# Optimization experiments

Hardware: AMD Instinct MI355X
Metric: run time of the kernel (lower is better)

The kernel has to match this reference:

```python
import jax, jax.numpy as jnp
import numpy as np

B, T, D, H, J = 64, 128, 768, 256, 128  # batch, tokens, input_dim, span_hidden_dim, top_injection_dim
PRUNING_RATIO = 2.0


def setup_inputs() -> dict:
    key = jax.random.key(0)
    ks = jax.random.split(key, 12)
    def w(k, shape, fan_in):
        return jax.random.normal(k, shape, jnp.float32) / np.sqrt(fan_in)
    return {
        "inputs": jax.random.normal(ks[0], (B, T, D), jnp.float32),
        "input_mask": jnp.ones((B, T), jnp.int32),
        "top_injection_embedding": jax.random.normal(ks[1], (B, J), jnp.float32),
        # SpanRepAssembly: start / end projections
        "W_start": w(ks[2], (D, H), D), "b_start": jnp.zeros((H,), jnp.float32),
        "W_end": w(ks[3], (D, H), D), "b_end": jnp.zeros((H,), jnp.float32),
        # span_scorer: ReLU -> Linear(H,H) -> ReLU -> Linear(H,1)
        "W_s1": w(ks[4], (H, H), H), "b_s1": jnp.zeros((H,), jnp.float32),
        "W_s2": w(ks[5], (H, 1), H), "b_s2": jnp.zeros((1,), jnp.float32),
        # top injection path
        "W_inj": w(ks[6], (J, H), J), "b_inj": jnp.zeros((H,), jnp.float32),
        "W_sec": w(ks[7], (H, H), H), "b_sec": jnp.zeros((H,), jnp.float32),
        "W_pred": w(ks[8], (H, 1), H), "b_pred": jnp.zeros((1,), jnp.float32),
    }


def reference(inputs, input_mask, top_injection_embedding,
              W_start, b_start, W_end, b_end,
              W_s1, b_s1, W_s2, b_s2,
              W_inj, b_inj, W_sec, b_sec, W_pred, b_pred):
    b, t, _ = inputs.shape
    k_spans = int(PRUNING_RATIO * t)
    # SpanRepAssembly: span_hidden[b, (s,e)] = startProj(x_s) + endProj(x_e), s <= e,
    # flattened start-major (matches start_end_range ordering).
    A = inputs @ W_start + b_start                      # [B,T,H]
    E = inputs @ W_end + b_end                          # [B,T,H]
    s_idx, e_idx = jnp.triu_indices(t)                  # N = T(T+1)/2 spans, row-major
    span_hidden = A[:, s_idx] + E[:, e_idx]             # [B,N,H]
    m = input_mask.astype(jnp.float32)
    span_mask = m[:, s_idx] * m[:, e_idx]               # [B,N]
    # span_scorer MLP over all spans
    h = jax.nn.relu(span_hidden) @ W_s1 + b_s1
    scores = (jax.nn.relu(h) @ W_s2 + b_s2)[..., 0]     # [B,N]
    # SpanPruner: mask invalid spans to -inf, top-k, sort indices, gather
    masked_scores = jnp.where(span_mask > 0, scores, -jnp.inf)
    _, top_idx = jax.lax.top_k(masked_scores, k_spans)  # [B,K]
    top_idx = jnp.sort(top_idx, axis=1)
    top_span_hidden = jnp.take_along_axis(span_hidden, top_idx[:, :, None], axis=1)  # [B,K,H]
    top_span_mask = jnp.take_along_axis(span_mask, top_idx, axis=1)[..., None]       # [B,K,1]
    top_span_scores = jnp.take_along_axis(masked_scores, top_idx, axis=1)[..., None] # [B,K,1]
    top_span_scores = jnp.where(jnp.isinf(top_span_scores), -1.0, top_span_scores)
    # top-injection scoring head
    inj = (top_injection_embedding @ W_inj + b_inj)[:, None, :]      # [B,1,H]
    sec = top_span_hidden @ W_sec + b_sec                            # [B,K,H]
    top_span_logits = jax.nn.relu(inj + sec) @ W_pred + b_pred + top_span_scores  # [B,K,1]
    top_span_probs = jax.nn.sigmoid(top_span_logits) * top_span_mask
    return top_span_probs
```

## Files before the change

### kernel.cpp

```cpp
#include <hip/hip_runtime.h>
#include <hip/hip_bf16.h>
#include <math.h>

#define BB 64
#define T 128
#define DD 768
#define H 256
#define JJ 128
#define NSPAN 8256
#define KTOP 256
#define SCAP 1024
#define MARGIN 0.03f

typedef __attribute__((ext_vector_type(8))) short bf16x8;
typedef __attribute__((ext_vector_type(4))) float f32x4;

__device__ inline unsigned short bfrne(float x) {
    unsigned u = __float_as_uint(x);
    return (unsigned short)((u + 0x7FFFu + ((u >> 16) & 1u)) >> 16);
}

__device__ inline unsigned pk2(float x, float y) {
    float2 f; f.x = x; f.y = y;
    __hip_bfloat162 h = __float22bfloat162_rn(f);
    return *reinterpret_cast<unsigned*>(&h);
}

template<int CTRL>
__device__ __forceinline__ float dpp_add16(float v) {
    return v + __int_as_float(__builtin_amdgcn_update_dpp(
        0, __float_as_int(v), CTRL, 0xF, 0xF, true));
}

__global__ __launch_bounds__(256) void prep_proj_kernel(
    const float* __restrict__ X,
    const float* __restrict__ Wa, const float* __restrict__ ba,
    const float* __restrict__ Wb, const float* __restrict__ bb,
    float* __restrict__ AE,
    int* __restrict__ s_idx, int* __restrict__ e_idx,
    const float* __restrict__ W1, unsigned short* __restrict__ Wpk,
    const float* __restrict__ tie, const float* __restrict__ Winj,
    const float* __restrict__ binj, float* __restrict__ injv)
{
    const int blk = blockIdx.x;
    const int t = threadIdx.x;

    if (blk >= 256) {
        const int pblk = blk - 256;
        if (pblk == 0) {
            if (t < T) {
                int s = t;
                int start = s * T - (s * (s - 1)) / 2;
                int len = T - s;
                for (int i = 0; i < len; ++i) {
                    s_idx[start + i] = s;
                    e_idx[start + i] = s + i;
                }
            }
        } else if (pblk <= 256) {
            int idx = (pblk - 1) * 256 + t;
            int j  = idx & 7;
            int l  = (idx >> 3) & 63;
            int kc = (idx >> 9) & 7;
            int ct = idx >> 12;
            int k = kc * 32 + (l >> 4) * 8 + j;
            int n = ct * 16 + (l & 15);
            Wpk[idx] = bfrne(W1[k * 256 + n]);
        } else {
            int b = pblk - 257;
            __shared__ float tb[JJ];
            if (t < JJ) tb[t] = tie[b * JJ + t];
            __syncthreads();
            float a = binj[t];
            for (int j = 0; j < JJ; ++j)
                a = fmaf(tb[j], Winj[j * H + t], a);
            injv[b * H + t] = a;
        }
        return;
    }

    const int px = blk & 63;
    const int cb = blk >> 6;
    const int m0 = px * 128;
    const float* W    = (cb < 2) ? Wa : Wb;
    const float* bias = (cb < 2) ? ba : bb;
    const int wc0 = (cb & 1) * 128;
    const int oc0 = (cb < 2) ? wc0 : (256 + wc0);

    const int tx = t & 15;
    const int ty = t >> 4;
    const int r0 = m0 + ty * 8;
    const int c0 = wc0 + tx * 8;

    const float* Xb  = X + (size_t)r0 * DD;
    const float* Wc  = W + c0;

    float4 XA[8], WA[8], XB[8], WB[8];
    float acc[8][8];
#pragma unroll
    for (int i = 0; i < 8; ++i)
#pragma unroll
        for (int j = 0; j < 8; ++j) acc[i][j] = 0.f;

    auto loadX = [&](float4 (&xr)[8], int kb) {
        const int kk = kb * 4;
#pragma unroll
        for (int r = 0; r < 8; ++r)
            xr[r] = *(const float4*)&Xb[(size_t)r * DD + kk];
    };
    auto loadW = [&](float4 (&wr)[8], int kb) {
#pragma unroll
        for (int j = 0; j < 4; ++j) {
            const float* wp = &Wc[(size_t)(kb * 4 + j) * 256];
            wr[j * 2]     = *(const float4*)&wp[0];
            wr[j * 2 + 1] = *(const float4*)&wp[4];
        }
    };
    auto comp = [&](const float4 (&xr)[8], const float4 (&wr)[8]) {
#pragma unroll
        for (int j = 0; j < 4; ++j) {
            const float wq[8] = {wr[j*2].x, wr[j*2].y, wr[j*2].z, wr[j*2].w,
                                 wr[j*2+1].x, wr[j*2+1].y, wr[j*2+1].z, wr[j*2+1].w};
#pragma unroll
            for (int r = 0; r < 8; ++r) {
                const float xv = (j == 0) ? xr[r].x : (j == 1) ? xr[r].y
                               : (j == 2) ? xr[r].z : xr[r].w;
#pragma unroll
                for (int c = 0; c < 8; ++c)
                    acc[r][c] = fmaf(xv, wq[c], acc[r][c]);
            }
        }
    };

    loadX(XA, 0); loadW(WA, 0);
    for (int kb = 0; kb < 192; kb += 2) {
        loadX(XB, kb + 1); loadW(WB, kb + 1);
        comp(XA, WA);
        if (kb + 2 < 192) { loadX(XA, kb + 2); loadW(WA, kb + 2); }
        comp(XB, WB);
    }

    float bq[8];
#pragma unroll
    for (int j = 0; j < 8; ++j) bq[j] = bias[wc0 + tx * 8 + j];
#pragma unroll
    for (int r = 0; r < 8; ++r) {
        const size_t row = r0 + r;
        float4 o0, o1;
        o0.x = acc[r][0] + bq[0]; o0.y = acc[r][1] + bq[1];
        o0.z = acc[r][2] + bq[2]; o0.w = acc[r][3] + bq[3];
        o1.x = acc[r][4] + bq[4]; o1.y = acc[r][5] + bq[5];
        o1.z = acc[r][6] + bq[6]; o1.w = acc[r][7] + bq[7];
        *(float4*)&AE[row * 512 + oc0 + tx * 8]     = o0;
        *(float4*)&AE[row * 512 + oc0 + tx * 8 + 4] = o1;
    }
}

__global__ __launch_bounds__(512, 4) void approx_kernel(
    const float* __restrict__ AE,
    const unsigned short* __restrict__ Wpk,
    const float* __restrict__ bs1, const float* __restrict__ Ws2,
    const float* __restrict__ bs2g,
    const int* __restrict__ s_idx, const int* __restrict__ e_idx,
    const int* __restrict__ maskp,
    float* __restrict__ scores)
{
    const int bid   = blockIdx.x;
    const int r     = bid & 7;
    const int q     = bid >> 3;
    const int g     = q >> 3;
    const int chunk = q & 7;
    const int b     = g * 8 + r;
    const int tile0 = chunk * 65;
    const int tcnt  = (516 - tile0 < 65) ? (516 - tile0) : 65;

    __shared__ __align__(16) unsigned short rshf[2][8][64][8];
    __shared__ float pslice[2][8][16];

    const int t      = threadIdx.x;
    const int w      = t >> 6;
    const int lane   = t & 63;
    const int lrow16 = lane & 15;
    const int quad   = lane >> 4;

    bf16x8 bfr[2][8];
    float b1c[2], w2c[2];
#pragma unroll
    for (int c = 0; c < 2; ++c) {
#pragma unroll
        for (int kc = 0; kc < 8; ++kc)
            bfr[c][kc] = *(const bf16x8*)&Wpk[((((2 * w + c) * 8 + kc) * 64) + lane) * 8];
        int col = (2 * w + c) * 16 + lrow16;
        b1c[c] = bs1[col];
        w2c[c] = Ws2[col];
    }
    const float bs2v = bs2g[0];

    const float* Abase = AE + (size_t)b * T * 512;
    const int sp   = t >> 5;
    const int km   = t & 31;
    const int kc_s = km >> 2;
    const int q_s  = km & 3;
    const int slot = (q_s * 16 + sp + kc_s) & 63;

    {
        int n = tile0 * 16 + sp;
        int s = s_idx[n], e = e_idx[n];
        const float* Ar = Abase + (size_t)s * 512 + km * 8;
        const float* Er = Abase + (size_t)e * 512 + 256 + km * 8;
        float4 a0 = *(const float4*)&Ar[0];
        float4 a1 = *(const float4*)&Ar[4];
        float4 e0 = *(const float4*)&Er[0];
        float4 e1 = *(const float4*)&Er[4];
        uint4 v;
        v.x = pk2(fmaxf(a0.x + e0.x, 0.f), fmaxf(a0.y + e0.y, 0.f));
        v.y = pk2(fmaxf(a0.z + e0.z, 0.f), fmaxf(a0.w + e0.w, 0.f));
        v.z = pk2(fmaxf(a1.x + e1.x, 0.f), fmaxf(a1.y + e1.y, 0.f));
        v.w = pk2(fmaxf(a1.z + e1.z, 0.f), fmaxf(a1.w + e1.w, 0.f));
        *(uint4*)&rshf[0][kc_s][slot][0] = v;
    }
    int s_nx = 0, e_nx = 0;
    if (tcnt > 1) {
        int n = (tile0 + 1) * 16 + sp;
        s_nx = s_idx[n]; e_nx = e_idx[n];
    }
    __syncthreads();

    for (int tt = 0; tt < tcnt; ++tt) {
        const int cur = tt & 1;
        float4 a0, a1, e0, e1;
        const bool pf = (tt + 1 < tcnt);
        if (pf) {
            const float* Ar = Abase + (size_t)s_nx * 512 + km * 8;
            const float* Er = Abase + (size_t)e_nx * 512 + 256 + km * 8;
            a0 = *(const float4*)&Ar[0];
            a1 = *(const float4*)&Ar[4];
            e0 = *(const float4*)&Er[0];
            e1 = *(const float4*)&Er[4];
        }
        if (tt + 2 < tcnt) {
            int n = (tile0 + tt + 2) * 16 + sp;
            s_nx = s_idx[n]; e_nx = e_idx[n];
        }
        f32x4 acc0 = {0.f, 0.f, 0.f, 0.f};
        f32x4 acc1 = {0.f, 0.f, 0.f, 0.f};
#pragma unroll
        for (int kc = 0; kc < 8; ++kc) {
            bf16x8 a = *(const bf16x8*)&rshf[cur][kc][(lane + kc) & 63][0];
            acc0 = __builtin_amdgcn_mfma_f32_16x16x32_bf16(a, bfr[0][kc], acc0, 0, 0, 0);
            acc1 = __builtin_amdgcn_mfma_f32_16x16x32_bf16(a, bfr[1][kc], acc1, 0, 0, 0);
        }
        float ps[4];
#pragma unroll
        for (int rr = 0; rr < 4; ++rr)
            ps[rr] = fmaxf(acc0[rr] + b1c[0], 0.f) * w2c[0]
                   + fmaxf(acc1[rr] + b1c[1], 0.f) * w2c[1];
#pragma unroll
        for (int rr = 0; rr < 4; ++rr) {
            float v = ps[rr];
            v = dpp_add16<0xB1>(v);
            v = dpp_add16<0x4E>(v);
            v = dpp_add16<0x141>(v);
            v = dpp_add16<0x140>(v);
            ps[rr] = v;
        }
        if (lrow16 == 0) {
            float4 v; v.x = ps[0]; v.y = ps[1]; v.z = ps[2]; v.w = ps[3];
            *(float4*)&pslice[cur][w][quad * 4] = v;
        }
        if (pf) {
            uint4 v;
            v.x = pk2(fmaxf(a0.x + e0.x, 0.f), fmaxf(a0.y + e0.y, 0.f));
            v.y = pk2(fmaxf(a0.z + e0.z, 0.f), fmaxf(a0.w + e0.w, 0.f));
            v.z = pk2(fmaxf(a1.x + e1.x, 0.f), fmaxf(a1.y + e1.y, 0.f));
            v.w = pk2(fmaxf(a1.z + e1.z, 0.f), fmaxf(a1.w + e1.w, 0.f));
            *(uint4*)&rshf[cur ^ 1][kc_s][slot][0] = v;
        }
        __syncthreads();
        if (t < 16) {
            int n = (tile0 + tt) * 16 + t;
            float sc = bs2v;
#pragma unroll
            for (int ww = 0; ww < 8; ++ww) sc += pslice[cur][ww][t];
            int s = s_idx[n], e = e_idx[n];
            bool m = (maskp[b * T + s] != 0) && (maskp[b * T + e] != 0);
            scores[(size_t)b * NSPAN + n] = m ? sc : -INFINITY;
        }
    }
}

__global__ __launch_bounds__(1024) void select_kernel(
    const float* __restrict__ scores,
    int* __restrict__ shortlist, int* __restrict__ slcnt)
{
    const int b = blockIdx.x;
    const int t = threadIdx.x;
    __shared__ unsigned su[NSPAN];
    __shared__ int hist[256];
    __shared__ unsigned s_prefix;
    __shared__ int s_remaining;
    __shared__ int wave_keep[16];

    const float* sc = scores + (size_t)b * NSPAN;
    for (int i = t; i < NSPAN; i += 1024) {
        unsigned ub = __float_as_uint(sc[i]);
        su[i] = (ub & 0x80000000u) ? ~ub : (ub | 0x80000000u);
    }
    __syncthreads();

    unsigned prefix = 0;
    int remaining = KTOP;
    for (int d = 3; d >= 0; --d) {
        if (t < 256) hist[t] = 0;
        __syncthreads();
        const int sh = d * 8;
        for (int i = t; i < NSPAN; i += 1024) {
            unsigned u = su[i];
            bool match = (d == 3) || ((u >> (sh + 8)) == (prefix >> (sh + 8)));
            if (match) atomicAdd(&hist[(u >> sh) & 255], 1);
        }
        __syncthreads();
        if (t == 0) {
            int acc = 0, v = 255;
            for (; v > 0; --v) {
                int h = hist[v];
                if (acc + h >= remaining) break;
                acc += h;
            }
            s_prefix = prefix | ((unsigned)v << sh);
            s_remaining = remaining - acc;
        }
        __syncthreads();
        prefix = s_prefix;
        remaining = s_remaining;
        __syncthreads();
    }

    unsigned ub = (prefix & 0x80000000u) ? (prefix & 0x7FFFFFFFu) : ~prefix;
    float kthf = __uint_as_float(ub);
    float tau = kthf - MARGIN;
    unsigned tb = __float_as_uint(tau);
    unsigned ktau = (tb & 0x80000000u) ? ~tb : (tb | 0x80000000u);

    const int wid = t >> 6, lane = t & 63;
    int base = 0;
    const unsigned long long ltmask = (1ull << lane) - 1ull;
    for (int c0 = 0; c0 < NSPAN; c0 += 1024) {
        int n = c0 + t;
        bool keep = (n < NSPAN) && (su[n] >= ktau);
        unsigned long long bk = __ballot(keep);
        int before = __popcll(bk & ltmask);
        if (lane == 0) wave_keep[wid] = __popcll(bk);
        __syncthreads();
        int kb = base;
        for (int wv = 0; wv < wid; ++wv) kb += wave_keep[wv];
        if (keep) {
            int pos = kb + before;
            if (pos < SCAP) shortlist[b * SCAP + pos] = n;
        }
        for (int wv = 0; wv < 16; ++wv) base += wave_keep[wv];
        __syncthreads();
    }
    if (t == 0) slcnt[b] = base < SCAP ? base : SCAP;
}

__global__ __launch_bounds__(512) void exact_kernel(
    const float* __restrict__ AE,
    const float* __restrict__ Ws1, const float* __restrict__ bs1,
    const float* __restrict__ Ws2, const float* __restrict__ bs2g,
    const int* __restrict__ s_idx, const int* __restrict__ e_idx,
    const int* __restrict__ shortlist, const int* __restrict__ slcnt,
    float* __restrict__ scores)
{
    const int b  = blockIdx.y;
    const int n0 = blockIdx.x * 64;
    const int cntb = slcnt[b];
    if (n0 >= cntb) return;

    __shared__ float rsh[64][36];
    __shared__ float Ws[32][260];
    __shared__ int   ss[64], se[64], nn[64];

    const int t = threadIdx.x;
    if (t < 64) {
        int row = n0 + t;
        int n = 0;
        if (row < cntb) n = shortlist[b * SCAP + row];
        nn[t] = (row < cntb) ? n : -1;
        ss[t] = s_idx[n]; se[t] = e_idx[n];
    }
    __syncthreads();

    const int tx = t & 31;
    const int ty = t >> 5;
    float acc[4][8];
#pragma unroll
    for (int i = 0; i < 4; ++i)
#pragma unroll
        for (int j = 0; j < 8; ++j) acc[i][j] = 0.f;

    const float* Abase = AE + (size_t)b * T * 512;

    for (int kk = 0; kk < 256; kk += 32) {
        __syncthreads();
        {
            int row = t >> 4, q4 = (t & 15) * 4;
#pragma unroll
            for (int q = 0; q < 4; ++q)
                *(float4*)&Ws[row][q4 + q * 64] =
                    *(const float4*)&Ws1[(size_t)(kk + row) * 256 + q4 + q * 64];
        }
        {
            int sp = t >> 3, k4 = (t & 7) * 4;
            const float* Ar = Abase + (size_t)ss[sp] * 512 + kk + k4;
            const float* Er = Abase + (size_t)se[sp] * 512 + 256 + kk + k4;
            float4 a = *(const float4*)Ar;
            float4 e = *(const float4*)Er;
            float4 v;
            v.x = fmaxf(a.x + e.x, 0.f); v.y = fmaxf(a.y + e.y, 0.f);
            v.z = fmaxf(a.z + e.z, 0.f); v.w = fmaxf(a.w + e.w, 0.f);
            *(float4*)&rsh[sp][k4] = v;
        }
        __syncthreads();
#pragma unroll
        for (int k4 = 0; k4 < 32; k4 += 4) {
            float w[4][8];
#pragma unroll
            for (int kq = 0; kq < 4; ++kq) {
                float4 w0 = *(const float4*)&Ws[k4 + kq][tx * 4];
                float4 w1 = *(const float4*)&Ws[k4 + kq][128 + tx * 4];
                w[kq][0] = w0.x; w[kq][1] = w0.y; w[kq][2] = w0.z; w[kq][3] = w0.w;
                w[kq][4] = w1.x; w[kq][5] = w1.y; w[kq][6] = w1.z; w[kq][7] = w1.w;
            }
#pragma unroll
            for (int i = 0; i < 4; ++i) {
                float4 rv = *(const float4*)&rsh[ty * 4 + i][k4];
                float rq[4] = {rv.x, rv.y, rv.z, rv.w};
#pragma unroll
                for (int kq = 0; kq < 4; ++kq)
#pragma unroll
                    for (int j = 0; j < 8; ++j)
                        acc[i][j] = fmaf(rq[kq], w[kq][j], acc[i][j]);
            }
        }
    }

    float b1[8], w2[8];
#pragma unroll
    for (int j = 0; j < 8; ++j) {
        int c = (j < 4) ? (tx * 4 + j) : (128 + tx * 4 + j - 4);
        b1[j] = bs1[c];
        w2[j] = Ws2[c];
    }
    const float bs2v = bs2g[0];
#pragma unroll
    for (int i = 0; i < 4; ++i) {
        int r = ty * 4 + i;
        float p = 0.f;
#pragma unroll
        for (int j = 0; j < 8; ++j)
            p += fmaxf(acc[i][j] + b1[j], 0.f) * w2[j];
#pragma unroll
        for (int off = 16; off > 0; off >>= 1)
            p += __shfl_down(p, off, 32);
        if (tx == 0) {
            int n = nn[r];
            if (n >= 0)
                scores[(size_t)b * NSPAN + n] = p + bs2v;
        }
    }
}

__global__ __launch_bounds__(1024) void topk_kernel(
    const float* __restrict__ scores,
    const int* __restrict__ shortlist, const int* __restrict__ slcnt,
    int* __restrict__ top_idx, float* __restrict__ top_scores)
{
    const int b = blockIdx.x;
    const int t = threadIdx.x;
    const int cnt = slcnt[b];

    __shared__ unsigned su[SCAP];
    __shared__ int sn[SCAP];
    __shared__ int hist[256];
    __shared__ unsigned s_prefix;
    __shared__ int s_remaining;
    __shared__ int wave_eq[16], wave_keep[16];

    for (int i = t; i < cnt; i += 1024) {
        int n = shortlist[b * SCAP + i];
        unsigned ub = __float_as_uint(scores[(size_t)b * NSPAN + n]);
        su[i] = (ub & 0x80000000u) ? ~ub : (ub | 0x80000000u);
        sn[i] = n;
    }
    __syncthreads();

    unsigned prefix = 0;
    int remaining = KTOP;
    for (int d = 3; d >= 0; --d) {
        if (t < 256) hist[t] = 0;
        __syncthreads();
        const int sh = d * 8;
        for (int i = t; i < cnt; i += 1024) {
            unsigned u = su[i];
            bool match = (d == 3) || ((u >> (sh + 8)) == (prefix >> (sh + 8)));
            if (match) atomicAdd(&hist[(u >> sh) & 255], 1);
        }
        __syncthreads();
        if (t == 0) {
            int acc = 0, v = 255;
            for (; v > 0; --v) {
                int h = hist[v];
                if (acc + h >= remaining) break;
                acc += h;
            }
            s_prefix = prefix | ((unsigned)v << sh);
            s_remaining = remaining - acc;
        }
        __syncthreads();
        prefix = s_prefix;
        remaining = s_remaining;
        __syncthreads();
    }
    const unsigned v = prefix;
    const int need_eq = remaining;

    const int wid = t >> 6, lane = t & 63;
    int base_eq = 0, base_keep = 0;
    const unsigned long long ltmask = (1ull << lane) - 1ull;
    for (int c0 = 0; c0 < cnt; c0 += 1024) {
        int i = c0 + t;
        bool valid = i < cnt;
        unsigned u = valid ? su[i] : 0u;
        bool eq = valid && (u == v);
        bool gt = valid && (u > v);
        unsigned long long beq = __ballot(eq);
        int eq_before = __popcll(beq & ltmask);
        if (lane == 0) wave_eq[wid] = __popcll(beq);
        __syncthreads();
        int eqb = base_eq;
        for (int w = 0; w < wid; ++w) eqb += wave_eq[w];
        int eq_rank = eqb + eq_before;
        bool keep = gt || (eq && (eq_rank < need_eq));
        unsigned long long bk = __ballot(keep);
        int keep_before = __popcll(bk & ltmask);
        if (lane == 0) wave_keep[wid] = __popcll(bk);
        __syncthreads();
        int kb = base_keep;
        for (int w = 0; w < wid; ++w) kb += wave_keep[w];
        if (keep) {
            int pos = kb + keep_before;
            top_idx[b * KTOP + pos] = sn[i];
            unsigned fb = (u & 0x80000000u) ? (u & 0x7FFFFFFFu) : ~u;
            float f = __uint_as_float(fb);
            top_scores[b * KTOP + pos] = isinf(f) ? -1.0f : f;
        }
        for (int w = 0; w < 16; ++w) { base_eq += wave_eq[w]; base_keep += wave_keep[w]; }
        __syncthreads();
    }
}

__global__ __launch_bounds__(256) void final_kernel(
    const float* __restrict__ AE,
    const int* __restrict__ s_idx, const int* __restrict__ e_idx,
    const int* __restrict__ maskp,
    const int* __restrict__ top_idx, const float* __restrict__ top_scores,
    const float* __restrict__ injv,
    const float* __restrict__ Wsec, const float* __restrict__ bsec,
    const float* __restrict__ Wpred, const float* __restrict__ bpredg,
    float* __restrict__ out)
{
    const int b = blockIdx.x >> 2;
    const int k0 = (blockIdx.x & 3) * 64;

    __shared__ float sh[64][36];
    __shared__ float Ws[32][260];
    __shared__ int ss[64], se[64];
    __shared__ float msk[64], tsc[64];

    const int t = threadIdx.x;
    if (t < 64) {
        int kidx = k0 + t;
        int n = top_idx[b * KTOP + kidx];
        int s = s_idx[n], e = e_idx[n];
        ss[t] = s; se[t] = e;
        msk[t] = (maskp[b * T + s] != 0 && maskp[b * T + e] != 0) ? 1.f : 0.f;
        tsc[t] = top_scores[b * KTOP + kidx];
    }
    __syncthreads();

    const int tx = t & 31;
    const int ty = t >> 5;
    float acc[8][8];
#pragma unroll
    for (int i = 0; i < 8; ++i)
#pragma unroll
        for (int j = 0; j < 8; ++j) acc[i][j] = 0.f;

    const float* Abase = AE + (size_t)b * T * 512;

    for (int kk = 0; kk < 256; kk += 32) {
        __syncthreads();
        {
            int c4 = (t & 63) * 4, r0 = t >> 6;
#pragma unroll
            for (int r8 = 0; r8 < 8; ++r8) {
                int row = r0 + r8 * 4;
                *(float4*)&Ws[row][c4] =
                    *(const float4*)&Wsec[(size_t)(kk + row) * 256 + c4];
            }
        }
        {
            int sp = t >> 2, k8 = (t & 3) * 8;
            const float* Ar = Abase + (size_t)ss[sp] * 512 + kk + k8;
            const float* Er = Abase + (size_t)se[sp] * 512 + 256 + kk + k8;
#pragma unroll
            for (int q = 0; q < 2; ++q) {
                float4 a = *(const float4*)&Ar[q * 4];
                float4 e = *(const float4*)&Er[q * 4];
                float4 v;
                v.x = a.x + e.x; v.y = a.y + e.y; v.z = a.z + e.z; v.w = a.w + e.w;
                *(float4*)&sh[sp][k8 + q * 4] = v;
            }
        }
        __syncthreads();
#pragma unroll
        for (int k4 = 0; k4 < 32; k4 += 4) {
            float w[4][8];
#pragma unroll
            for (int kq = 0; kq < 4; ++kq) {
                float4 w0 = *(const float4*)&Ws[k4 + kq][tx * 4];
                float4 w1 = *(const float4*)&Ws[k4 + kq][128 + tx * 4];
                w[kq][0] = w0.x; w[kq][1] = w0.y; w[kq][2] = w0.z; w[kq][3] = w0.w;
                w[kq][4] = w1.x; w[kq][5] = w1.y; w[kq][6] = w1.z; w[kq][7] = w1.w;
            }
#pragma unroll
            for (int i = 0; i < 8; ++i) {
                float4 rv = *(const float4*)&sh[ty * 8 + i][k4];
                float rq[4] = {rv.x, rv.y, rv.z, rv.w};
#pragma unroll
                for (int kq = 0; kq < 4; ++kq)
#pragma unroll
                    for (int j = 0; j < 8; ++j)
                        acc[i][j] = fmaf(rq[kq], w[kq][j], acc[i][j]);
            }
        }
    }

    float bsec_r[8], wpred_r[8], injr[8];
#pragma unroll
    for (int j = 0; j < 8; ++j) {
        int c = (j < 4) ? (tx * 4 + j) : (128 + tx * 4 + j - 4);
        bsec_r[j] = bsec[c];
        wpred_r[j] = Wpred[c];
        injr[j] = injv[b * H + c];
    }
    const float bp = bpredg[0];
#pragma unroll
    for (int i = 0; i < 8; ++i) {
        int r = ty * 8 + i;
        float p = 0.f;
#pragma unroll
        for (int j = 0; j < 8; ++j) {
            float sec = acc[i][j] + bsec_r[j];
            p += fmaxf(injr[j] + sec, 0.f) * wpred_r[j];
        }
#pragma unroll
        for (int off = 16; off > 0; off >>= 1)
            p += __shfl_down(p, off, 32);
        if (tx == 0) {
            float logit = p + bp + tsc[r];
            float prob = (1.f / (1.f + expf(-logit))) * msk[r];
            out[b * KTOP + k0 + r] = prob;
        }
    }
}

extern "C" void kernel_launch(void* const* d_in, const int* in_sizes, int n_in,
                              void* d_out, int out_size, void* d_ws, size_t ws_size,
                              hipStream_t stream) {
    const float* inputs  = (const float*)d_in[0];
    const int*   imask   = (const int*)d_in[1];
    const float* tie     = (const float*)d_in[2];
    const float* W_start = (const float*)d_in[3];
    const float* b_start = (const float*)d_in[4];
    const float* W_end   = (const float*)d_in[5];
    const float* b_end   = (const float*)d_in[6];
    const float* W_s1    = (const float*)d_in[7];
    const float* b_s1    = (const float*)d_in[8];
    const float* W_s2    = (const float*)d_in[9];
    const float* b_s2    = (const float*)d_in[10];
    const float* W_inj   = (const float*)d_in[11];
    const float* b_inj   = (const float*)d_in[12];
    const float* W_sec   = (const float*)d_in[13];
    const float* b_sec   = (const float*)d_in[14];
    const float* W_pred  = (const float*)d_in[15];
    const float* b_pred  = (const float*)d_in[16];
    float* out = (float*)d_out;

    float* AE         = (float*)d_ws;
    float* scores     = AE + (size_t)BB * T * 512;
    int*   s_idx      = (int*)(scores + (size_t)BB * NSPAN);
    int*   e_idx      = s_idx + NSPAN;
    int*   top_idx    = e_idx + NSPAN;
    float* top_scores = (float*)(top_idx + BB * KTOP);
    float* injv       = top_scores + BB * KTOP;
    unsigned short* Wpk = (unsigned short*)(injv + BB * H);
    int*   shortlist  = (int*)(Wpk + 65536);
    int*   slcnt      = shortlist + BB * SCAP;

    prep_proj_kernel<<<577, 256, 0, stream>>>(inputs, W_start, b_start, W_end, b_end, AE,
                                              s_idx, e_idx, W_s1, Wpk,
                                              tie, W_inj, b_inj, injv);
    approx_kernel<<<512, 512, 0, stream>>>(AE, Wpk, b_s1, W_s2, b_s2,
                                           s_idx, e_idx, imask, scores);
    select_kernel<<<BB, 1024, 0, stream>>>(scores, shortlist, slcnt);
    exact_kernel<<<dim3(16, BB), 512, 0, stream>>>(AE, W_s1, b_s1, W_s2, b_s2,
                                                   s_idx, e_idx, shortlist, slcnt, scores);
    topk_kernel<<<BB, 1024, 0, stream>>>(scores, shortlist, slcnt, top_idx, top_scores);
    final_kernel<<<BB * 4, 256, 0, stream>>>(AE, s_idx, e_idx, imask, top_idx, top_scores,
                                             injv, W_sec, b_sec, W_pred, b_pred, out);
}
```

Measured before the change: 477.7 us.

## Stage projection weights in shared memory and halve the column tile per block

Result: slower. 591.1 us (+23.7%).

```diff
diff --git a/kernel.cpp b/kernel.cpp
--- a/kernel.cpp
+++ b/kernel.cpp
@@ -45,8 +45,8 @@
     const int blk = blockIdx.x;
     const int t = threadIdx.x;
 
-    if (blk >= 256) {
-        const int pblk = blk - 256;
+    if (blk >= 512) {
+        const int pblk = blk - 512;
         if (pblk == 0) {
             if (t < T) {
                 int s = t;
@@ -80,79 +80,91 @@
     }
 
     const int px = blk & 63;
-    const int cb = blk >> 6;
+    const int cw = blk >> 6;
     const int m0 = px * 128;
-    const float* W    = (cb < 2) ? Wa : Wb;
-    const float* bias = (cb < 2) ? ba : bb;
-    const int wc0 = (cb & 1) * 128;
-    const int oc0 = (cb < 2) ? wc0 : (256 + wc0);
+    const float* W    = (cw < 4) ? Wa : Wb;
+    const float* bias = (cw < 4) ? ba : bb;
+    const int c0w = (cw & 3) * 64;
+    const int oc0 = (cw < 4) ? c0w : (256 + c0w);
 
     const int tx = t & 15;
     const int ty = t >> 4;
     const int r0 = m0 + ty * 8;
-    const int c0 = wc0 + tx * 8;
-
-    const float* Xb  = X + (size_t)r0 * DD;
-    const float* Wc  = W + c0;
-
-    float4 XA[8], WA[8], XB[8], WB[8];
-    float acc[8][8];
-#pragma unroll
-    for (int i = 0; i < 8; ++i)
-#pragma unroll
-        for (int j = 0; j < 8; ++j) acc[i][j] = 0.f;
-
-    auto loadX = [&](float4 (&xr)[8], int kb) {
-        const int kk = kb * 4;
+
+    __shared__ __align__(16) float Wt[32][64];
+
+    const float* Xb = X + (size_t)r0 * DD;
+
+    const int wrow = t >> 3;
+    const int wcol = (t & 7) * 8;
+
+    float4 wst[2];
+    auto loadWst = [&](int it) {
+        const float* wp = &W[(size_t)(it * 32 + wrow) * 256 + c0w + wcol];
+        wst[0] = *(const float4*)&wp[0];
+        wst[1] = *(const float4*)&wp[4];
+    };
+
+    float4 XA[8], XB[8];
+    auto loadX = [&](float4 (&xr)[8], int g) {
+        const int kk = g * 4;
 #pragma unroll
         for (int r = 0; r < 8; ++r)
             xr[r] = *(const float4*)&Xb[(size_t)r * DD + kk];
     };
-    auto loadW = [&](float4 (&wr)[8], int kb) {
+
+    float acc[8][4];
+#pragma unroll
+    for (int r = 0; r < 8; ++r)
+#pragma unroll
+        for (int c = 0; c < 4; ++c) acc[r][c] = 0.f;
+
+    auto comp = [&](const float4 (&xr)[8], int kb) {
 #pragma unroll
         for (int j = 0; j < 4; ++j) {
-            const float* wp = &Wc[(size_t)(kb * 4 + j) * 256];
-            wr[j * 2]     = *(const float4*)&wp[0];
-            wr[j * 2 + 1] = *(const float4*)&wp[4];
-        }
-    };
-    auto comp = [&](const float4 (&xr)[8], const float4 (&wr)[8]) {
-#pragma unroll
-        for (int j = 0; j < 4; ++j) {
-            const float wq[8] = {wr[j*2].x, wr[j*2].y, wr[j*2].z, wr[j*2].w,
-                                 wr[j*2+1].x, wr[j*2+1].y, wr[j*2+1].z, wr[j*2+1].w};
+            const float4 wv = *(const float4*)&Wt[kb * 4 + j][tx * 4];
 #pragma unroll
             for (int r = 0; r < 8; ++r) {
                 const float xv = (j == 0) ? xr[r].x : (j == 1) ? xr[r].y
                                : (j == 2) ? xr[r].z : xr[r].w;
-#pragma unroll
-                for (int c = 0; c < 8; ++c)
-                    acc[r][c] = fmaf(xv, wq[c], acc[r][c]);
+                acc[r][0] = fmaf(xv, wv.x, acc[r][0]);
+                acc[r][1] = fmaf(xv, wv.y, acc[r][1]);
+                acc[r][2] = fmaf(xv, wv.z, acc[r][2]);
+                acc[r][3] = fmaf(xv, wv.w, acc[r][3]);
             }
         }
     };
 
-    loadX(XA, 0); loadW(WA, 0);
-    for (int kb = 0; kb < 192; kb += 2) {
-        loadX(XB, kb + 1); loadW(WB, kb + 1);
-        comp(XA, WA);
-        if (kb + 2 < 192) { loadX(XA, kb + 2); loadW(WA, kb + 2); }
-        comp(XB, WB);
-    }
-
-    float bq[8];
-#pragma unroll
-    for (int j = 0; j < 8; ++j) bq[j] = bias[wc0 + tx * 8 + j];
+    loadWst(0);
+    loadX(XA, 0);
+
+    for (int it = 0; it < 24; ++it) {
+        __syncthreads();
+        *(float4*)&Wt[wrow][wcol]     = wst[0];
+        *(float4*)&Wt[wrow][wcol + 4] = wst[1];
+        __syncthreads();
+        if (it + 1 < 24) loadWst(it + 1);
+        const int g0 = it * 8;
+#pragma unroll
+        for (int kb = 0; kb < 8; kb += 2) {
+            const int g = g0 + kb;
+            if (g + 1 < 192) loadX(XB, g + 1);
+            comp(XA, kb);
+            if (g + 2 < 192) loadX(XA, g + 2);
+            comp(XB, kb + 1);
+        }
+    }
+
+    float bq[4];
+#pragma unroll
+    for (int j = 0; j < 4; ++j) bq[j] = bias[c0w + tx * 4 + j];
 #pragma unroll
     for (int r = 0; r < 8; ++r) {
         const size_t row = r0 + r;
-        float4 o0, o1;
-        o0.x = acc[r][0] + bq[0]; o0.y = acc[r][1] + bq[1];
-        o0.z = acc[r][2] + bq[2]; o0.w = acc[r][3] + bq[3];
-        o1.x = acc[r][4] + bq[4]; o1.y = acc[r][5] + bq[5];
-        o1.z = acc[r][6] + bq[6]; o1.w = acc[r][7] + bq[7];
-        *(float4*)&AE[row * 512 + oc0 + tx * 8]     = o0;
-        *(float4*)&AE[row * 512 + oc0 + tx * 8 + 4] = o1;
+        float4 o;
+        o.x = acc[r][0] + bq[0]; o.y = acc[r][1] + bq[1];
+        o.z = acc[r][2] + bq[2]; o.w = acc[r][3] + bq[3];
+        *(float4*)&AE[row * 512 + oc0 + tx * 4] = o;
     }
 }
 
@@ -709,7 +721,7 @@
     int*   shortlist  = (int*)(Wpk + 65536);
     int*   slcnt      = shortlist + BB * SCAP;
 
-    prep_proj_kernel<<<577, 256, 0, stream>>>(inputs, W_start, b_start, W_end, b_end, AE,
+    prep_proj_kernel<<<833, 256, 0, stream>>>(inputs, W_start, b_start, W_end, b_end, AE,
                                               s_idx, e_idx, W_s1, Wpk,
                                               tie, W_inj, b_inj, injv);
     approx_kernel<<<512, 512, 0, stream>>>(AE, Wpk, b_s1, W_s2, b_s2,
```
